# Performance work log

Measured on AMD Instinct MI355X. Metric: run time of the kernel, lower is better.

Reference implementation:

```python
import jax, jax.numpy as jnp
import numpy as np

N_NODES = 100000
N_EDGES = 1600000
MIN_NORM = 1e-15
EPS_F32 = 4e-3  # PoincareBall eps for float32


def _norm(x):
    return jnp.clip(jnp.linalg.norm(x, axis=-1, keepdims=True), MIN_NORM)


def artanh(x):
    x = jnp.clip(x, -1.0 + 1e-15, 1.0 - 1e-15)
    return 0.5 * (jnp.log1p(x) - jnp.log1p(-x))


def proj(x, c):
    norm = _norm(x)
    maxnorm = (1.0 - EPS_F32) / jnp.sqrt(c)
    return jnp.where(norm > maxnorm, x / norm * maxnorm, x)


def expmap0(u, c):
    sqrt_c = jnp.sqrt(c)
    u_norm = _norm(u)
    return jnp.tanh(sqrt_c * u_norm) * u / (sqrt_c * u_norm)


def logmap0(p, c):
    sqrt_c = jnp.sqrt(c)
    p_norm = _norm(p)
    return artanh(sqrt_c * p_norm) * p / (sqrt_c * p_norm)


def mobius_add(x, y, c):
    x2 = jnp.sum(x * x, axis=-1, keepdims=True)
    y2 = jnp.sum(y * y, axis=-1, keepdims=True)
    xy = jnp.sum(x * y, axis=-1, keepdims=True)
    num = (1.0 + 2.0 * c * xy + c * y2) * x + (1.0 - c * x2) * y
    denom = 1.0 + 2.0 * c * xy + (c ** 2) * x2 * y2
    return num / jnp.clip(denom, MIN_NORM)


def mobius_matvec(m, x, c):
    sqrt_c = jnp.sqrt(c)
    x_norm = _norm(x)
    mx = x @ m.T  # [N, out]
    mx_norm = _norm(mx)
    res = jnp.tanh(mx_norm / x_norm * artanh(sqrt_c * x_norm)) * mx / (mx_norm * sqrt_c)
    cond = jnp.all(mx == 0.0, axis=-1, keepdims=True)
    return jnp.where(cond, 0.0, res)


def hyp_linear(x, w, b, c):
    mv = proj(mobius_matvec(w, x, c), c)
    hyp_bias = proj(expmap0(b[None, :], c), c)  # proj_tan0 is identity on Poincare ball
    return proj(mobius_add(mv, hyp_bias, c), c)


def hyp_agg(x, edge_row, edge_col, edge_weight, c):
    x_tan = logmap0(x, c)
    msgs = edge_weight[:, None] * x_tan[edge_col]  # gather source features
    support = jax.ops.segment_sum(msgs, edge_row, num_segments=N_NODES)
    return proj(expmap0(support, c), c)


def hyp_act(x, c_in, c_out):
    xt = jax.nn.relu(logmap0(x, c_in))  # proj_tan0 identity
    return proj(expmap0(xt, c_out), c_out)


def setup_inputs() -> dict:
    key = jax.random.key(0)
    ks = jax.random.split(key, 10)
    x = jax.random.normal(ks[0], (N_NODES, 1433), dtype=jnp.float32)
    edge_row = jax.random.randint(ks[1], (N_EDGES,), 0, N_NODES, dtype=jnp.int32)
    edge_col = jax.random.randint(ks[2], (N_EDGES,), 0, N_NODES, dtype=jnp.int32)
    edge_weight = jax.random.uniform(ks[3], (N_EDGES,), dtype=jnp.float32)
    w1 = jax.random.normal(ks[4], (100, 1433), dtype=jnp.float32) * 0.05
    b1 = jax.random.normal(ks[5], (100,), dtype=jnp.float32) * 0.05
    w2 = jax.random.normal(ks[6], (64, 100), dtype=jnp.float32) * 0.05
    b2 = jax.random.normal(ks[7], (64,), dtype=jnp.float32) * 0.05
    lin_w = jax.random.normal(ks[8], (7, 64), dtype=jnp.float32) * 0.05
    lin_b = jax.random.normal(ks[9], (7,), dtype=jnp.float32) * 0.05
    return {"x": x, "edge_row": edge_row, "edge_col": edge_col,
            "edge_weight": edge_weight, "w1": w1, "b1": b1,
            "w2": w2, "b2": b2, "lin_w": lin_w, "lin_b": lin_b}


def reference(x, edge_row, edge_col, edge_weight, w1, b1, w2, b2, lin_w, lin_b):
    c = 1.0
    # encode: tangent -> hyperbolic (proj_tan0 is identity)
    h = proj(expmap0(x, c), c)
    # layer 1: HypLinear -> HypAgg -> HypAct
    h = hyp_linear(h, w1, b1, c)
    h = hyp_agg(h, edge_row, edge_col, edge_weight, c)
    h = hyp_act(h, c, c)
    # layer 2
    h = hyp_linear(h, w2, b2, c)
    h = hyp_agg(h, edge_row, edge_col, edge_weight, c)
    h = hyp_act(h, c, c)
    # decode: logmap0 -> Linear(64,7) with relu -> log_softmax
    t = logmap0(h, c)
    logits = jax.nn.relu(t @ lin_w.T + lin_b)
    return jax.nn.log_softmax(logits, axis=-1)
```

## Files before the change

kernel.cpp:

```cpp
#include <hip/hip_runtime.h>
#include <hip/hip_bf16.h>
#include <math.h>

#define MINN 1e-15f
#define MAXN 0.996f

#define KPAD 1472

typedef __attribute__((ext_vector_type(8))) short short8;
typedef __attribute__((ext_vector_type(4))) float f32x4;

__device__ __forceinline__ float artanhf_(float v){
  v = fminf(fmaxf(v, -0.9999999f), 0.9999999f);
  return 0.5f*(log1pf(v) - log1pf(-v));
}
__device__ __forceinline__ float grp8(float v){
  v += __shfl_xor(v,1,8); v += __shfl_xor(v,2,8); v += __shfl_xor(v,4,8); return v;
}
__device__ __forceinline__ float grp16w(float v){
  v += __shfl_xor(v,1,16); v += __shfl_xor(v,2,16);
  v += __shfl_xor(v,4,16); v += __shfl_xor(v,8,16); return v;
}
__device__ __forceinline__ unsigned short f2bf(float f){
  unsigned int u = __float_as_uint(f);
  unsigned int r = (u + 0x7fffu + ((u >> 16) & 1u)) >> 16;
  return (unsigned short)r;
}
__device__ __forceinline__ float bf2f(unsigned short h){
  return __uint_as_float(((unsigned int)h) << 16);
}
__device__ __forceinline__ unsigned short f2bf_c(float f){
  __hip_bfloat16 b = __float2bfloat16(f);
  return *reinterpret_cast<unsigned short*>(&b);
}

typedef __attribute__((address_space(1))) const unsigned int gu32;
typedef __attribute__((address_space(3))) unsigned int su32;
__device__ __forceinline__ void gload_lds16(const void* g, void* s){
  __builtin_amdgcn_global_load_lds((gu32*)g, (su32*)s, 16, 0, 0);
}

__global__ __launch_bounds__(256) void k_prep(const float* __restrict__ w1,
    const float* __restrict__ b1, const float* __restrict__ b2,
    unsigned short* __restrict__ w1hi,
    float* __restrict__ hb1, float* __restrict__ hb2, float* __restrict__ scal,
    int* __restrict__ counts, int N){
  int idx = blockIdx.x*256 + threadIdx.x;
  if (idx < 112*KPAD){
    int col = idx / KPAD, k = idx - col*KPAD;
    float v = (col < 100 && k < 1433) ? w1[(size_t)col*1433 + k] : 0.f;
    w1hi[idx] = f2bf(v);
  }
  if (idx < N) counts[idx] = 0;

  if (blockIdx.x == 0){
    __shared__ float red[128];
    int t = threadIdx.x;
    float v = (t < 100) ? b1[t] : 0.f;
    if (t < 128) red[t] = v*v;
    __syncthreads();
    for (int s=64;s;s>>=1){ if (t<s) red[t]+=red[t+s]; __syncthreads(); }
    float n2 = red[0]; __syncthreads();
    float n = fmaxf(sqrtf(n2), MINN);
    float s1 = tanhf(n)/n;
    float pn = fmaxf(tanhf(n), MINN);
    float t1 = pn > MAXN ? MAXN/pn : 1.f;
    float hv = s1*t1*v;
    if (t < 128) hb1[t] = (t<100) ? hv : 0.f;
    if (t < 128) red[t] = (t<100) ? hv*hv : 0.f;
    __syncthreads();
    for (int s=64;s;s>>=1){ if (t<s) red[t]+=red[t+s]; __syncthreads(); }
    if (t==0) scal[0] = red[0];
    __syncthreads();
    float v2 = (t < 64) ? b2[t] : 0.f;
    if (t < 128) red[t] = v2*v2;
    __syncthreads();
    for (int s=64;s;s>>=1){ if (t<s) red[t]+=red[t+s]; __syncthreads(); }
    float n2b = red[0]; __syncthreads();
    float nb = fmaxf(sqrtf(n2b), MINN);
    float s1b = tanhf(nb)/nb;
    float pnb = fmaxf(tanhf(nb), MINN);
    float t1b = pnb > MAXN ? MAXN/pnb : 1.f;
    float hvb = s1b*t1b*v2;
    if (t < 64) hb2[t] = hvb;
    if (t < 128) red[t] = (t<64) ? hvb*hvb : 0.f;
    __syncthreads();
    for (int s=64;s;s>>=1){ if (t<s) red[t]+=red[t+s]; __syncthreads(); }
    if (t==0) scal[1] = red[0];
  }
}

__global__ __launch_bounds__(512) void k_lin1_mfma(
    const float* __restrict__ x, const unsigned short* __restrict__ w1hi,
    const float* __restrict__ hb1,
    const float* __restrict__ scal, unsigned short* __restrict__ xtan1, int N,
    const int* __restrict__ er, int* __restrict__ counts, int E)
{
  __shared__ alignas(16) char bsm[2*14*1024];
  int tid = threadIdx.x;

  {
    int gsz = gridDim.x * 512;
    for (int e = blockIdx.x*512 + tid; e < E; e += gsz)
      atomicAdd(&counts[er[e]], 1);
  }

  int w = tid >> 6, l = tid & 63;
  int lr = l & 15, lg = l >> 4;
  int bm = blockIdx.x * 128;
  int row0 = bm + w*16;
  int r = row0 + lr;
  const float* xr = x + (size_t)min(r, N-1)*1433 + lg*8;
  float b1sq = scal[0];

  f32x4 acc[7];
  #pragma unroll
  for (int t=0;t<7;t++) acc[t] = (f32x4){0.f,0.f,0.f,0.f};
  float sq = 0.f;

  auto stage = [&](int buf, int kbase){
    #pragma unroll
    for (int c = 0; c < 2; ++c){
      int cc = w + 8*c;
      if (cc < 14){
        int h = (cc >= 7) ? 1 : 0;
        int t = cc - h*7;
        const unsigned short* src = w1hi + (size_t)(t*16 + lr)*KPAD + kbase + h*32 + lg*8;
        gload_lds16(src, bsm + (buf*14 + cc)*1024);
      }
    }
  };
  auto xload = [&](float* d, int kbase){
    #pragma unroll
    for (int h = 0; h < 2; ++h){
      int kk = kbase + h*32;
      const float* p = xr + kk;
      if (kk + 32 <= 1433) {
        #pragma unroll
        for (int j=0;j<8;j++) d[h*8+j] = p[j];
      } else {
        #pragma unroll
        for (int j=0;j<8;j++){
          bool kv = (kk + lg*8 + j) < 1433;
          d[h*8+j] = kv ? p[j] : 0.f;
        }
      }
    }
  };

  stage(0, 0);
  float xa[16];
  xload(xa, 0);
  __syncthreads();

  for (int kb = 0; kb < 23; ++kb) {
    int cur = kb & 1, nxt = cur ^ 1;
    int nk = (kb + 1) * 64;

    float xb[16];
    if (kb + 1 < 23){
      stage(nxt, nk);
      xload(xb, nk);
    } else {
      #pragma unroll
      for (int j=0;j<16;j++) xb[j] = 0.f;
    }

    #pragma unroll
    for (int h = 0; h < 2; ++h){
      short8 ah, al;
      #pragma unroll
      for (int j=0;j<8;j++){
        float v = xa[h*8+j];
        sq = fmaf(v, v, sq);
        unsigned short hu = f2bf_c(v);
        ah[j] = (short)hu;
        float hf = bf2f(hu);
        al[j] = (short)f2bf_c(v - hf);
      }
      const char* base = bsm + (cur*14 + h*7)*1024 + (l << 4);
      short8 bh[7];
      #pragma unroll
      for (int t=0;t<7;t++)
        bh[t] = *reinterpret_cast<const short8*>(base + t*1024);
      #pragma unroll
      for (int t=0;t<7;t++){
        acc[t] = __builtin_amdgcn_mfma_f32_16x16x32_bf16(ah, bh[t], acc[t], 0,0,0);
        acc[t] = __builtin_amdgcn_mfma_f32_16x16x32_bf16(al, bh[t], acc[t], 0,0,0);
      }
    }
    #pragma unroll
    for (int j=0;j<16;j++) xa[j] = xb[j];

    __syncthreads();
  }

  sq += __shfl_xor(sq, 16); sq += __shfl_xor(sq, 32);

  float hbv[7];
  #pragma unroll
  for (int t=0;t<7;t++) hbv[t] = hb1[t*16 + lr];

  #pragma unroll
  for (int r4=0;r4<4;r4++){
    int rrow = 4*lg + r4;
    float v[7];
    #pragma unroll
    for (int t=0;t<7;t++) v[t] = acc[t][r4];
    float yn2 = 0.f, dotb = 0.f;
    #pragma unroll
    for (int t=0;t<7;t++){ yn2 += v[t]*v[t]; dotb += v[t]*hbv[t]; }
    yn2 = grp16w(yn2); dotb = grp16w(dotb);
    float xn2 = __shfl(sq, rrow);

    float un = fmaxf(sqrtf(xn2), MINN);
    float th = tanhf(un);
    float sE = th/un;
    float pn = fmaxf(th, MINN);
    float t1 = pn > MAXN ? MAXN/pn : 1.f;
    float gam = sE*t1;
    float xh = fmaxf(gam*un, MINN);
    float yn = sqrtf(yn2);
    float mxn = fmaxf(gam*yn, MINN);
    float rs = tanhf(mxn/xh*artanhf_(xh))/mxn;
    if (yn2 == 0.f) rs = 0.f;
    float rn = rs*gam*yn;
    float t2 = rn > MAXN ? MAXN/fmaxf(rn,MINN) : 1.f;
    float alpha = t2*rs*gam;
    float x2v = alpha*alpha*yn2;
    float xyv = alpha*dotb;
    float den = fmaxf(1.f + 2.f*xyv + x2v*b1sq, MINN);
    float A = (1.f + 2.f*xyv + b1sq)/den, B = (1.f - x2v)/den;
    float Aa = A*alpha;
    float on2 = 0.f;
    float o[7];
    #pragma unroll
    for (int t=0;t<7;t++){ o[t] = Aa*v[t] + B*hbv[t]; on2 += o[t]*o[t]; }
    on2 = grp16w(on2);
    float on = sqrtf(on2);
    float onc = fmaxf(on, MINN);
    float t3 = onc > MAXN ? MAXN/onc : 1.f;
    float pn3 = fmaxf(t3*on, MINN);
    float fs = artanhf_(pn3)/pn3 * t3;

    int grow = row0 + rrow;
    if (grow < N){
      #pragma unroll
      for (int t=0;t<7;t++){
        int c = t*16 + lr;
        if (c < 100) xtan1[(size_t)grow*100 + c] = f2bf(fs*o[t]);
      }
    }
  }
}

__global__ __launch_bounds__(256) void k_scan1(const int* __restrict__ counts, int* __restrict__ row_start,
                                               int* __restrict__ blksum, int N){
  __shared__ int s[256];
  int t = threadIdx.x;
  int base = blockIdx.x*1024 + t*4;
  int v[4]; int sum = 0;
  #pragma unroll
  for (int i=0;i<4;i++){ v[i] = (base+i < N) ? counts[base+i] : 0; sum += v[i]; }
  s[t] = sum; __syncthreads();
  for (int off=1; off<256; off<<=1){
    int val = (t >= off) ? s[t-off] : 0;
    __syncthreads();
    s[t] += val;
    __syncthreads();
  }
  int run = (t > 0) ? s[t-1] : 0;
  #pragma unroll
  for (int i=0;i<4;i++){ if (base+i < N) row_start[base+i] = run; run += v[i]; }
  if (t == 255) blksum[blockIdx.x] = s[255];
}

__global__ __launch_bounds__(256) void k_scan3(int* __restrict__ row_start, const int* __restrict__ blksum,
                                               int* __restrict__ cursor, int N){
  __shared__ int pref;
  if (threadIdx.x == 0){
    int seg = blockIdx.x >> 2;
    int s = 0;
    for (int q = 0; q < seg; ++q) s += blksum[q];
    pref = s;
  }
  __syncthreads();
  int i = blockIdx.x*256 + threadIdx.x;
  if (i < N){ int v = row_start[i] + pref; row_start[i] = v; cursor[i] = v; }
}

__global__ __launch_bounds__(256) void k_scatter(const int* __restrict__ er, const int* __restrict__ ec,
    const float* __restrict__ ew, int* __restrict__ cursor,
    uint2* __restrict__ meta, int E){
  int e = blockIdx.x*256 + threadIdx.x;
  if (e < E){
    int r = er[e];
    int pos = atomicAdd(&cursor[r], 1);
    uint2 m;
    m.x = (unsigned int)ec[e];
    m.y = __float_as_uint(ew[e]);
    meta[pos] = m;
  }
}

__global__ __launch_bounds__(256) void k_agg100(
    const unsigned short* __restrict__ xt, const int* __restrict__ row_start,
    const int* __restrict__ counts, const uint2* __restrict__ meta,
    float* __restrict__ sup, int N)
{
  int row = blockIdx.x*4 + (threadIdx.x >> 6);
  int lane = threadIdx.x & 63;
  if (row >= N) return;
  int start = row_start[row], cnt = counts[row];
  bool act = lane < 50;
  float a0 = 0.f, a1 = 0.f;
  for (int j = 0; j < cnt; j += 64) {
    int cc = 0; float wt = 0.f;
    if (j + lane < cnt) { uint2 m = meta[start + j + lane]; cc = (int)m.x; wt = __uint_as_float(m.y); }
    int lim = min(64, cnt - j);
    int k = 0;
    for (; k + 8 <= lim; k += 8) {
      const unsigned int *p0,*p1,*p2,*p3,*p4,*p5,*p6,*p7;
      float w0,w1,w2,w3,w4,w5,w6,w7;
      p0 = reinterpret_cast<const unsigned int*>(xt + (size_t)__shfl(cc,k+0)*100); w0 = __shfl(wt,k+0);
      p1 = reinterpret_cast<const unsigned int*>(xt + (size_t)__shfl(cc,k+1)*100); w1 = __shfl(wt,k+1);
      p2 = reinterpret_cast<const unsigned int*>(xt + (size_t)__shfl(cc,k+2)*100); w2 = __shfl(wt,k+2);
      p3 = reinterpret_cast<const unsigned int*>(xt + (size_t)__shfl(cc,k+3)*100); w3 = __shfl(wt,k+3);
      p4 = reinterpret_cast<const unsigned int*>(xt + (size_t)__shfl(cc,k+4)*100); w4 = __shfl(wt,k+4);
      p5 = reinterpret_cast<const unsigned int*>(xt + (size_t)__shfl(cc,k+5)*100); w5 = __shfl(wt,k+5);
      p6 = reinterpret_cast<const unsigned int*>(xt + (size_t)__shfl(cc,k+6)*100); w6 = __shfl(wt,k+6);
      p7 = reinterpret_cast<const unsigned int*>(xt + (size_t)__shfl(cc,k+7)*100); w7 = __shfl(wt,k+7);
      if (act){
        unsigned int u0=p0[lane],u1=p1[lane],u2=p2[lane],u3=p3[lane];
        unsigned int u4=p4[lane],u5=p5[lane],u6=p6[lane],u7=p7[lane];
        a0 += w0*bf2f((unsigned short)u0); a1 += w0*bf2f((unsigned short)(u0>>16));
        a0 += w1*bf2f((unsigned short)u1); a1 += w1*bf2f((unsigned short)(u1>>16));
        a0 += w2*bf2f((unsigned short)u2); a1 += w2*bf2f((unsigned short)(u2>>16));
        a0 += w3*bf2f((unsigned short)u3); a1 += w3*bf2f((unsigned short)(u3>>16));
        a0 += w4*bf2f((unsigned short)u4); a1 += w4*bf2f((unsigned short)(u4>>16));
        a0 += w5*bf2f((unsigned short)u5); a1 += w5*bf2f((unsigned short)(u5>>16));
        a0 += w6*bf2f((unsigned short)u6); a1 += w6*bf2f((unsigned short)(u6>>16));
        a0 += w7*bf2f((unsigned short)u7); a1 += w7*bf2f((unsigned short)(u7>>16));
      }
    }
    for (; k < lim; ++k) {
      int col = __shfl(cc, k);
      float w_  = __shfl(wt, k);
      if (act){
        unsigned int u = reinterpret_cast<const unsigned int*>(xt + (size_t)col*100)[lane];
        a0 += w_*bf2f((unsigned short)u);
        a1 += w_*bf2f((unsigned short)(u>>16));
      }
    }
  }
  if (act){
    float2* dst = reinterpret_cast<float2*>(sup + (size_t)row*100);
    dst[lane] = make_float2(a0, a1);
  }
}

__global__ __launch_bounds__(256) void k_agg64(
    const unsigned short* __restrict__ xt, const int* __restrict__ row_start,
    const int* __restrict__ counts, const uint2* __restrict__ meta,
    float* __restrict__ sup, int N)
{
  int row = blockIdx.x*4 + (threadIdx.x >> 6);
  int lane = threadIdx.x & 63;
  if (row >= N) return;
  int half = lane >> 5, sl = lane & 31;
  int start = row_start[row], cnt = counts[row];
  float a0 = 0.f, a1 = 0.f;
  for (int j = 0; j < cnt; j += 64) {
    int cc = 0; float wt = 0.f;
    if (j + lane < cnt) { uint2 m = meta[start + j + lane]; cc = (int)m.x; wt = __uint_as_float(m.y); }
    int lim = min(64, cnt - j);
    int k = 0;
    for (; k + 16 <= lim; k += 16) {
      const unsigned int *p0,*p1,*p2,*p3,*p4,*p5,*p6,*p7;
      float w0,w1,w2,w3,w4,w5,w6,w7;
      p0 = reinterpret_cast<const unsigned int*>(xt + (size_t)__shfl(cc,k+ 0+half)*64); w0 = __shfl(wt,k+ 0+half);
      p1 = reinterpret_cast<const unsigned int*>(xt + (size_t)__shfl(cc,k+ 2+half)*64); w1 = __shfl(wt,k+ 2+half);
      p2 = reinterpret_cast<const unsigned int*>(xt + (size_t)__shfl(cc,k+ 4+half)*64); w2 = __shfl(wt,k+ 4+half);
      p3 = reinterpret_cast<const unsigned int*>(xt + (size_t)__shfl(cc,k+ 6+half)*64); w3 = __shfl(wt,k+ 6+half);
      p4 = reinterpret_cast<const unsigned int*>(xt + (size_t)__shfl(cc,k+ 8+half)*64); w4 = __shfl(wt,k+ 8+half);
      p5 = reinterpret_cast<const unsigned int*>(xt + (size_t)__shfl(cc,k+10+half)*64); w5 = __shfl(wt,k+10+half);
      p6 = reinterpret_cast<const unsigned int*>(xt + (size_t)__shfl(cc,k+12+half)*64); w6 = __shfl(wt,k+12+half);
      p7 = reinterpret_cast<const unsigned int*>(xt + (size_t)__shfl(cc,k+14+half)*64); w7 = __shfl(wt,k+14+half);
      unsigned int u0=p0[sl],u1=p1[sl],u2=p2[sl],u3=p3[sl];
      unsigned int u4=p4[sl],u5=p5[sl],u6=p6[sl],u7=p7[sl];
      a0 += w0*bf2f((unsigned short)u0); a1 += w0*bf2f((unsigned short)(u0>>16));
      a0 += w1*bf2f((unsigned short)u1); a1 += w1*bf2f((unsigned short)(u1>>16));
      a0 += w2*bf2f((unsigned short)u2); a1 += w2*bf2f((unsigned short)(u2>>16));
      a0 += w3*bf2f((unsigned short)u3); a1 += w3*bf2f((unsigned short)(u3>>16));
      a0 += w4*bf2f((unsigned short)u4); a1 += w4*bf2f((unsigned short)(u4>>16));
      a0 += w5*bf2f((unsigned short)u5); a1 += w5*bf2f((unsigned short)(u5>>16));
      a0 += w6*bf2f((unsigned short)u6); a1 += w6*bf2f((unsigned short)(u6>>16));
      a0 += w7*bf2f((unsigned short)u7); a1 += w7*bf2f((unsigned short)(u7>>16));
    }
    for (; k + 2 <= lim; k += 2) {
      int e = k + half;
      int col = __shfl(cc, e);
      float w_ = __shfl(wt, e);
      unsigned int u = reinterpret_cast<const unsigned int*>(xt + (size_t)col*64)[sl];
      a0 += w_*bf2f((unsigned short)u);
      a1 += w_*bf2f((unsigned short)(u>>16));
    }
    if (k < lim) {
      int col = __shfl(cc, k);
      float w_ = __shfl(wt, k);
      if (half == 0){
        unsigned int u = reinterpret_cast<const unsigned int*>(xt + (size_t)col*64)[sl];
        a0 += w_*bf2f((unsigned short)u);
        a1 += w_*bf2f((unsigned short)(u>>16));
      }
    }
  }
  a0 += __shfl_xor(a0, 32);
  a1 += __shfl_xor(a1, 32);
  if (lane < 32){
    float2* dst = reinterpret_cast<float2*>(sup + (size_t)row*64);
    dst[sl] = make_float2(a0, a1);
  }
}

__global__ __launch_bounds__(256) void k_layer2(
    const float* __restrict__ sup, const float* __restrict__ w2,
    const float* __restrict__ hb2, const float* __restrict__ scal,
    unsigned short* __restrict__ xtan2, int N)
{
  __shared__ alignas(16) float w2s[64][100];
  __shared__ float xts[32][105];
  __shared__ float hbs[64];
  int tid = threadIdx.x;
  for (int i = tid; i < 1600; i += 256)
    reinterpret_cast<float4*>(&w2s[0][0])[i] = reinterpret_cast<const float4*>(w2)[i];
  if (tid < 64) hbs[tid] = hb2[tid];
  float b2sq = scal[1];
  __syncthreads();
  int rr = tid >> 3, g = tid & 7;
  int grow = blockIdx.x*32 + rr;
  bool valid = grow < N;
  float sv[13]; float sn2 = 0.f;
  #pragma unroll
  for (int m=0;m<13;m++){
    int j = g + 8*m;
    float v = (valid && j < 100) ? sup[(size_t)grow*100 + j] : 0.f;
    sv[m] = v; sn2 += v*v;
  }
  sn2 = grp8(sn2);
  float snn = fmaxf(sqrtf(sn2), MINN);
  float e1 = tanhf(snn)/snn;
  float pnA = fmaxf(tanhf(snn), MINN);
  float t1 = pnA > MAXN ? MAXN/pnA : 1.f;
  float phi = e1*t1;
  float hn = fmaxf(phi*snn, MINN);
  float lam = artanhf_(hn)/hn;
  float xn2 = 0.f;
  #pragma unroll
  for (int m=0;m<13;m++){
    int j = g + 8*m;
    if (j < 100){ float v = fmaxf(lam*phi*sv[m], 0.f); xts[rr][j] = v; xn2 += v*v; }
  }
  xn2 = grp8(xn2);
  float xn = fmaxf(sqrtf(xn2), MINN);
  float e2 = tanhf(xn)/xn;
  float pnB = fmaxf(tanhf(xn), MINN);
  float t2 = pnB > MAXN ? MAXN/pnB : 1.f;
  float psi = e2*t2;
  __syncthreads();
  float z[8] = {};
  for (int j=0;j<100;j++){
    float xv = xts[rr][j];
    #pragma unroll
    for (int m=0;m<8;m++) z[m] += xv * w2s[g+8*m][j];
  }
  float zn2 = 0.f, dz = 0.f;
  #pragma unroll
  for (int m=0;m<8;m++){ zn2 += z[m]*z[m]; dz += z[m]*hbs[g+8*m]; }
  zn2 = grp8(zn2); dz = grp8(dz);
  float xnh = fmaxf(psi*xn, MINN);
  float zn = sqrtf(zn2);
  float mxn = fmaxf(psi*zn, MINN);
  float rs = tanhf(mxn/xnh*artanhf_(xnh))/mxn;
  if (zn2 == 0.f) rs = 0.f;
  float rn = rs*psi*zn;
  float t3 = rn > MAXN ? MAXN/fmaxf(rn,MINN) : 1.f;
  float alpha = t3*rs*psi;
  float x2 = alpha*alpha*zn2;
  float xy = alpha*dz;
  float den = fmaxf(1.f + 2.f*xy + x2*b2sq, MINN);
  float A = (1.f + 2.f*xy + b2sq)/den, B = (1.f - x2)/den;
  float Aa = A*alpha;
  float ov[8]; float on2 = 0.f;
  #pragma unroll
  for (int m=0;m<8;m++){ ov[m] = Aa*z[m] + B*hbs[g+8*m]; on2 += ov[m]*ov[m]; }
  on2 = grp8(on2);
  float on = sqrtf(on2);
  float onc = fmaxf(on, MINN);
  float t4 = onc > MAXN ? MAXN/onc : 1.f;
  float pn4 = fmaxf(t4*on, MINN);
  float fs = artanhf_(pn4)/pn4 * t4;
  if (valid)
    #pragma unroll
    for (int m=0;m<8;m++) xtan2[(size_t)grow*64 + g + 8*m] = f2bf(fs*ov[m]);
}

__global__ __launch_bounds__(256) void k_decode(
    const float* __restrict__ sup2, const float* __restrict__ lw,
    const float* __restrict__ lb, float* __restrict__ out, int N)
{
  __shared__ float lws[7][64];
  __shared__ float lbs[7];
  int tid = threadIdx.x;
  for (int i = tid; i < 448; i += 256) lws[i>>6][i&63] = lw[i];
  if (tid < 7) lbs[tid] = lb[tid];
  __syncthreads();
  int rr = tid >> 3, g = tid & 7;
  int grow = blockIdx.x*32 + rr;
  bool valid = grow < N;
  float sv[8]; float sn2 = 0.f;
  #pragma unroll
  for (int m=0;m<8;m++){
    int j = g + 8*m;
    float v = valid ? sup2[(size_t)grow*64 + j] : 0.f;
    sv[m] = v; sn2 += v*v;
  }
  sn2 = grp8(sn2);
  float snn = fmaxf(sqrtf(sn2), MINN);
  float e1 = tanhf(snn)/snn;
  float pnA = fmaxf(tanhf(snn), MINN);
  float t1 = pnA > MAXN ? MAXN/pnA : 1.f;
  float phi = e1*t1;
  float hn = fmaxf(phi*snn, MINN);
  float lam = artanhf_(hn)/hn;
  float xt[8]; float xn2 = 0.f;
  #pragma unroll
  for (int m=0;m<8;m++){ xt[m] = fmaxf(lam*phi*sv[m], 0.f); xn2 += xt[m]*xt[m]; }
  xn2 = grp8(xn2);
  float xn = fmaxf(sqrtf(xn2), MINN);
  float e2 = tanhf(xn)/xn;
  float pnB = fmaxf(tanhf(xn), MINN);
  float t2 = pnB > MAXN ? MAXN/pnB : 1.f;
  float psi = e2*t2;
  float tn = fmaxf(psi*xn, MINN);
  float lam2 = artanhf_(tn)/tn;
  float tc = lam2*psi;
  float lg[7];
  #pragma unroll
  for (int k=0;k<7;k++){
    float p = 0.f;
    #pragma unroll
    for (int m=0;m<8;m++) p += xt[m]*lws[k][g+8*m];
    p = grp8(p) * tc;
    lg[k] = fmaxf(p + lbs[k], 0.f);
  }
  float mx = lg[0];
  #pragma unroll
  for (int k=1;k<7;k++) mx = fmaxf(mx, lg[k]);
  float se = 0.f;
  #pragma unroll
  for (int k=0;k<7;k++) se += expf(lg[k]-mx);
  float lse = logf(se);
  if (valid && g < 7) out[(size_t)grow*7 + g] = lg[g] - mx - lse;
}

extern "C" void kernel_launch(void* const* d_in, const int* in_sizes, int n_in,
                              void* d_out, int out_size, void* d_ws, size_t ws_size,
                              hipStream_t stream)
{
  const float* x  = (const float*)d_in[0];
  const int*   er = (const int*)  d_in[1];
  const int*   ec = (const int*)  d_in[2];
  const float* ew = (const float*)d_in[3];
  const float* w1 = (const float*)d_in[4];
  const float* b1 = (const float*)d_in[5];
  const float* w2 = (const float*)d_in[6];
  const float* b2 = (const float*)d_in[7];
  const float* lw = (const float*)d_in[8];
  const float* lb = (const float*)d_in[9];
  float* out = (float*)d_out;
  int N = in_sizes[0] / 1433;
  int E = in_sizes[1];

  float* W = (float*)d_ws;
  float* hb1  = W;
  float* hb2  = W + 128;
  float* scal = W + 192;
  unsigned short* w1hi = (unsigned short*)(W + 256);
  uint2* meta = (uint2*)(W + 82688);
  int*   counts    = (int*)(W + 82688 + 2*(size_t)E);
  int*   row_start = counts + N;
  int*   cursor    = row_start + N;
  int*   blksum    = cursor + N;
  unsigned short* xtanb = (unsigned short*)(blksum + 128);
  float* sup = (float*)(xtanb + (size_t)N*100);

  int nblk_scan = (N + 1023) / 1024;
  int nb128 = (N + 127)/128;
  int nbg = (N + 3)/4;
  int nb32 = (N + 31)/32;

  k_prep<<<(112*KPAD + 255)/256, 256, 0, stream>>>(w1, b1, b2, w1hi, hb1, hb2, scal, counts, N);
  k_lin1_mfma<<<nb128, 512, 0, stream>>>(x, w1hi, hb1, scal, xtanb, N, er, counts, E);
  k_scan1<<<nblk_scan, 256, 0, stream>>>(counts, row_start, blksum, N);
  k_scan3<<<(N + 255)/256, 256, 0, stream>>>(row_start, blksum, cursor, N);
  k_scatter<<<(E + 255)/256, 256, 0, stream>>>(er, ec, ew, cursor, meta, E);
  k_agg100<<<nbg, 256, 0, stream>>>(xtanb, row_start, counts, meta, sup, N);
  k_layer2<<<nb32, 256, 0, stream>>>(sup, w2, hb2, scal, xtanb, N);
  k_agg64<<<nbg, 256, 0, stream>>>(xtanb, row_start, counts, meta, sup, N);
  k_decode<<<nb32, 256, 0, stream>>>(sup, lw, lb, out, N);
}
```

Measured before the change: 577.0 us.

## Process two rows per wavefront in aggregation kernels and reorder GEMM prefetch loads

Both SpMM aggregation kernels now assign two destination rows to each wavefront, with each half-wave loading the edge metadata for one row. The agg64 kernel gives each 32-lane half its own row, which removes the cross-half reduction. The agg100 kernel interleaves gathers for both rows to raise the number of loads in flight. This aims to reduce per-row overhead and improve memory-level parallelism, at the cost of imbalance when the two rows have different degrees. The layer-1 GEMM loop also issues the global x loads before the LDS staging of weights.

```diff
diff --git a/kernel.cpp b/kernel.cpp
--- a/kernel.cpp
+++ b/kernel.cpp
@@ -148,9 +148,9 @@
     }
   };
 
-  stage(0, 0);
   float xa[16];
   xload(xa, 0);
+  stage(0, 0);
   __syncthreads();
 
   for (int kb = 0; kb < 23; ++kb) {
@@ -159,8 +159,8 @@
 
     float xb[16];
     if (kb + 1 < 23){
+      xload(xb, nk);
       stage(nxt, nk);
-      xload(xb, nk);
     } else {
       #pragma unroll
       for (int j=0;j<16;j++) xb[j] = 0.f;
@@ -308,54 +308,81 @@
     const int* __restrict__ counts, const uint2* __restrict__ meta,
     float* __restrict__ sup, int N)
 {
-  int row = blockIdx.x*4 + (threadIdx.x >> 6);
+  int wv = threadIdx.x >> 6;
   int lane = threadIdx.x & 63;
-  if (row >= N) return;
-  int start = row_start[row], cnt = counts[row];
+  int pair = blockIdx.x*4 + wv;
+  int rowA = pair*2;
+  if (rowA >= N) return;
+  int rowB = rowA + 1;
+  bool hasB = rowB < N;
+  int sl = lane & 31, half = lane >> 5;
+  int startA = row_start[rowA], cntA = counts[rowA];
+  int startB = hasB ? row_start[rowB] : 0;
+  int cntB   = hasB ? counts[rowB] : 0;
   bool act = lane < 50;
-  float a0 = 0.f, a1 = 0.f;
-  for (int j = 0; j < cnt; j += 64) {
+  float a0=0.f, a1=0.f, b0=0.f, b1=0.f;
+  int cmax = max(cntA, cntB);
+
+  for (int j = 0; j < cmax; j += 32) {
     int cc = 0; float wt = 0.f;
-    if (j + lane < cnt) { uint2 m = meta[start + j + lane]; cc = (int)m.x; wt = __uint_as_float(m.y); }
-    int lim = min(64, cnt - j);
+    int myStart = half ? startB : startA;
+    int myCnt   = half ? cntB   : cntA;
+    if (j + sl < myCnt){ uint2 m = meta[myStart + j + sl]; cc = (int)m.x; wt = __uint_as_float(m.y); }
+    int limA = min(32, cntA - j);
+    int limB = min(32, cntB - j);
+    int limJ = min(limA, limB);
     int k = 0;
-    for (; k + 8 <= lim; k += 8) {
-      const unsigned int *p0,*p1,*p2,*p3,*p4,*p5,*p6,*p7;
-      float w0,w1,w2,w3,w4,w5,w6,w7;
-      p0 = reinterpret_cast<const unsigned int*>(xt + (size_t)__shfl(cc,k+0)*100); w0 = __shfl(wt,k+0);
-      p1 = reinterpret_cast<const unsigned int*>(xt + (size_t)__shfl(cc,k+1)*100); w1 = __shfl(wt,k+1);
-      p2 = reinterpret_cast<const unsigned int*>(xt + (size_t)__shfl(cc,k+2)*100); w2 = __shfl(wt,k+2);
-      p3 = reinterpret_cast<const unsigned int*>(xt + (size_t)__shfl(cc,k+3)*100); w3 = __shfl(wt,k+3);
-      p4 = reinterpret_cast<const unsigned int*>(xt + (size_t)__shfl(cc,k+4)*100); w4 = __shfl(wt,k+4);
-      p5 = reinterpret_cast<const unsigned int*>(xt + (size_t)__shfl(cc,k+5)*100); w5 = __shfl(wt,k+5);
-      p6 = reinterpret_cast<const unsigned int*>(xt + (size_t)__shfl(cc,k+6)*100); w6 = __shfl(wt,k+6);
-      p7 = reinterpret_cast<const unsigned int*>(xt + (size_t)__shfl(cc,k+7)*100); w7 = __shfl(wt,k+7);
+    for (; k + 4 <= limJ; k += 4) {
+      const unsigned int *pa0,*pa1,*pa2,*pa3,*pb0,*pb1,*pb2,*pb3;
+      float wa0,wa1,wa2,wa3,wb0,wb1,wb2,wb3;
+      pa0 = reinterpret_cast<const unsigned int*>(xt + (size_t)__shfl(cc,k+0)*100); wa0 = __shfl(wt,k+0);
+      pa1 = reinterpret_cast<const unsigned int*>(xt + (size_t)__shfl(cc,k+1)*100); wa1 = __shfl(wt,k+1);
+      pa2 = reinterpret_cast<const unsigned int*>(xt + (size_t)__shfl(cc,k+2)*100); wa2 = __shfl(wt,k+2);
+      pa3 = reinterpret_cast<const unsigned int*>(xt + (size_t)__shfl(cc,k+3)*100); wa3 = __shfl(wt,k+3);
+      pb0 = reinterpret_cast<const unsigned int*>(xt + (size_t)__shfl(cc,32+k+0)*100); wb0 = __shfl(wt,32+k+0);
+      pb1 = reinterpret_cast<const unsigned int*>(xt + (size_t)__shfl(cc,32+k+1)*100); wb1 = __shfl(wt,32+k+1);
+      pb2 = reinterpret_cast<const unsigned int*>(xt + (size_t)__shfl(cc,32+k+2)*100); wb2 = __shfl(wt,32+k+2);
+      pb3 = reinterpret_cast<const unsigned int*>(xt + (size_t)__shfl(cc,32+k+3)*100); wb3 = __shfl(wt,32+k+3);
       if (act){
-        unsigned int u0=p0[lane],u1=p1[lane],u2=p2[lane],u3=p3[lane];
-        unsigned int u4=p4[lane],u5=p5[lane],u6=p6[lane],u7=p7[lane];
-        a0 += w0*bf2f((unsigned short)u0); a1 += w0*bf2f((unsigned short)(u0>>16));
-        a0 += w1*bf2f((unsigned short)u1); a1 += w1*bf2f((unsigned short)(u1>>16));
-        a0 += w2*bf2f((unsigned short)u2); a1 += w2*bf2f((unsigned short)(u2>>16));
-        a0 += w3*bf2f((unsigned short)u3); a1 += w3*bf2f((unsigned short)(u3>>16));
-        a0 += w4*bf2f((unsigned short)u4); a1 += w4*bf2f((unsigned short)(u4>>16));
-        a0 += w5*bf2f((unsigned short)u5); a1 += w5*bf2f((unsigned short)(u5>>16));
-        a0 += w6*bf2f((unsigned short)u6); a1 += w6*bf2f((unsigned short)(u6>>16));
-        a0 += w7*bf2f((unsigned short)u7); a1 += w7*bf2f((unsigned short)(u7>>16));
-      }
-    }
-    for (; k < lim; ++k) {
-      int col = __shfl(cc, k);
-      float w_  = __shfl(wt, k);
+        unsigned int uA0=pa0[lane],uA1=pa1[lane],uA2=pa2[lane],uA3=pa3[lane];
+        unsigned int uB0=pb0[lane],uB1=pb1[lane],uB2=pb2[lane],uB3=pb3[lane];
+        a0 += wa0*bf2f((unsigned short)uA0); a1 += wa0*bf2f((unsigned short)(uA0>>16));
+        a0 += wa1*bf2f((unsigned short)uA1); a1 += wa1*bf2f((unsigned short)(uA1>>16));
+        a0 += wa2*bf2f((unsigned short)uA2); a1 += wa2*bf2f((unsigned short)(uA2>>16));
+        a0 += wa3*bf2f((unsigned short)uA3); a1 += wa3*bf2f((unsigned short)(uA3>>16));
+        b0 += wb0*bf2f((unsigned short)uB0); b1 += wb0*bf2f((unsigned short)(uB0>>16));
+        b0 += wb1*bf2f((unsigned short)uB1); b1 += wb1*bf2f((unsigned short)(uB1>>16));
+        b0 += wb2*bf2f((unsigned short)uB2); b1 += wb2*bf2f((unsigned short)(uB2>>16));
+        b0 += wb3*bf2f((unsigned short)uB3); b1 += wb3*bf2f((unsigned short)(uB3>>16));
+      }
+    }
+    int kA = k, kB = k;
+    for (; kA < limA; ++kA) {
+      int col = __shfl(cc, kA);
+      float w_ = __shfl(wt, kA);
       if (act){
         unsigned int u = reinterpret_cast<const unsigned int*>(xt + (size_t)col*100)[lane];
         a0 += w_*bf2f((unsigned short)u);
         a1 += w_*bf2f((unsigned short)(u>>16));
       }
     }
+    for (; kB < limB; ++kB) {
+      int col = __shfl(cc, 32+kB);
+      float w_ = __shfl(wt, 32+kB);
+      if (act){
+        unsigned int u = reinterpret_cast<const unsigned int*>(xt + (size_t)col*100)[lane];
+        b0 += w_*bf2f((unsigned short)u);
+        b1 += w_*bf2f((unsigned short)(u>>16));
+      }
+    }
   }
   if (act){
-    float2* dst = reinterpret_cast<float2*>(sup + (size_t)row*100);
-    dst[lane] = make_float2(a0, a1);
+    float2* dstA = reinterpret_cast<float2*>(sup + (size_t)rowA*100);
+    dstA[lane] = make_float2(a0, a1);
+    if (hasB){
+      float2* dstB = reinterpret_cast<float2*>(sup + (size_t)rowB*100);
+      dstB[lane] = make_float2(b0, b1);
+    }
   }
 }
 
@@ -364,28 +391,37 @@
     const int* __restrict__ counts, const uint2* __restrict__ meta,
     float* __restrict__ sup, int N)
 {
-  int row = blockIdx.x*4 + (threadIdx.x >> 6);
+  int wv = threadIdx.x >> 6;
   int lane = threadIdx.x & 63;
-  if (row >= N) return;
+  int pair = blockIdx.x*4 + wv;
+  int rowA = pair*2;
+  if (rowA >= N) return;
+  int rowB = rowA + 1;
+  bool hasB = rowB < N;
   int half = lane >> 5, sl = lane & 31;
-  int start = row_start[row], cnt = counts[row];
+  int myRow = half ? rowB : rowA;
+  bool live = (half == 0) || hasB;
+  int myStart = 0, myCnt = 0;
+  if (live){ myStart = row_start[myRow]; myCnt = counts[myRow]; }
   float a0 = 0.f, a1 = 0.f;
-  for (int j = 0; j < cnt; j += 64) {
+
+  for (int j = 0; j < myCnt; j += 32) {
     int cc = 0; float wt = 0.f;
-    if (j + lane < cnt) { uint2 m = meta[start + j + lane]; cc = (int)m.x; wt = __uint_as_float(m.y); }
-    int lim = min(64, cnt - j);
+    if (j + sl < myCnt){ uint2 m = meta[myStart + j + sl]; cc = (int)m.x; wt = __uint_as_float(m.y); }
+    int lim = min(32, myCnt - j);
+    int hb = half*32;
     int k = 0;
-    for (; k + 16 <= lim; k += 16) {
+    for (; k + 8 <= lim; k += 8) {
       const unsigned int *p0,*p1,*p2,*p3,*p4,*p5,*p6,*p7;
       float w0,w1,w2,w3,w4,w5,w6,w7;
-      p0 = reinterpret_cast<const unsigned int*>(xt + (size_t)__shfl(cc,k+ 0+half)*64); w0 = __shfl(wt,k+ 0+half);
-      p1 = reinterpret_cast<const unsigned int*>(xt + (size_t)__shfl(cc,k+ 2+half)*64); w1 = __shfl(wt,k+ 2+half);
-      p2 = reinterpret_cast<const unsigned int*>(xt + (size_t)__shfl(cc,k+ 4+half)*64); w2 = __shfl(wt,k+ 4+half);
-      p3 = reinterpret_cast<const unsigned int*>(xt + (size_t)__shfl(cc,k+ 6+half)*64); w3 = __shfl(wt,k+ 6+half);
-      p4 = reinterpret_cast<const unsigned int*>(xt + (size_t)__shfl(cc,k+ 8+half)*64); w4 = __shfl(wt,k+ 8+half);
-      p5 = reinterpret_cast<const unsigned int*>(xt + (size_t)__shfl(cc,k+10+half)*64); w5 = __shfl(wt,k+10+half);
-      p6 = reinterpret_cast<const unsigned int*>(xt + (size_t)__shfl(cc,k+12+half)*64); w6 = __shfl(wt,k+12+half);
-      p7 = reinterpret_cast<const unsigned int*>(xt + (size_t)__shfl(cc,k+14+half)*64); w7 = __shfl(wt,k+14+half);
+      p0 = reinterpret_cast<const unsigned int*>(xt + (size_t)__shfl(cc,hb+k+0)*64); w0 = __shfl(wt,hb+k+0);
+      p1 = reinterpret_cast<const unsigned int*>(xt + (size_t)__shfl(cc,hb+k+1)*64); w1 = __shfl(wt,hb+k+1);
+      p2 = reinterpret_cast<const unsigned int*>(xt + (size_t)__shfl(cc,hb+k+2)*64); w2 = __shfl(wt,hb+k+2);
+      p3 = reinterpret_cast<const unsigned int*>(xt + (size_t)__shfl(cc,hb+k+3)*64); w3 = __shfl(wt,hb+k+3);
+      p4 = reinterpret_cast<const unsigned int*>(xt + (size_t)__shfl(cc,hb+k+4)*64); w4 = __shfl(wt,hb+k+4);
+      p5 = reinterpret_cast<const unsigned int*>(xt + (size_t)__shfl(cc,hb+k+5)*64); w5 = __shfl(wt,hb+k+5);
+      p6 = reinterpret_cast<const unsigned int*>(xt + (size_t)__shfl(cc,hb+k+6)*64); w6 = __shfl(wt,hb+k+6);
+      p7 = reinterpret_cast<const unsigned int*>(xt + (size_t)__shfl(cc,hb+k+7)*64); w7 = __shfl(wt,hb+k+7);
       unsigned int u0=p0[sl],u1=p1[sl],u2=p2[sl],u3=p3[sl];
       unsigned int u4=p4[sl],u5=p5[sl],u6=p6[sl],u7=p7[sl];
       a0 += w0*bf2f((unsigned short)u0); a1 += w0*bf2f((unsigned short)(u0>>16));
@@ -397,28 +433,16 @@
       a0 += w6*bf2f((unsigned short)u6); a1 += w6*bf2f((unsigned short)(u6>>16));
       a0 += w7*bf2f((unsigned short)u7); a1 += w7*bf2f((unsigned short)(u7>>16));
     }
-    for (; k + 2 <= lim; k += 2) {
-      int e = k + half;
-      int col = __shfl(cc, e);
-      float w_ = __shfl(wt, e);
+    for (; k < lim; ++k) {
+      int col = __shfl(cc, hb+k);
+      float w_ = __shfl(wt, hb+k);
       unsigned int u = reinterpret_cast<const unsigned int*>(xt + (size_t)col*64)[sl];
       a0 += w_*bf2f((unsigned short)u);
       a1 += w_*bf2f((unsigned short)(u>>16));
     }
-    if (k < lim) {
-      int col = __shfl(cc, k);
-      float w_ = __shfl(wt, k);
-      if (half == 0){
-        unsigned int u = reinterpret_cast<const unsigned int*>(xt + (size_t)col*64)[sl];
-        a0 += w_*bf2f((unsigned short)u);
-        a1 += w_*bf2f((unsigned short)(u>>16));
-      }
-    }
-  }
-  a0 += __shfl_xor(a0, 32);
-  a1 += __shfl_xor(a1, 32);
-  if (lane < 32){
-    float2* dst = reinterpret_cast<float2*>(sup + (size_t)row*64);
+  }
+  if (live){
+    float2* dst = reinterpret_cast<float2*>(sup + (size_t)myRow*64);
     dst[sl] = make_float2(a0, a1);
   }
 }
@@ -597,7 +621,8 @@
 
   int nblk_scan = (N + 1023) / 1024;
   int nb128 = (N + 127)/128;
-  int nbg = (N + 3)/4;
+  int npair = (N + 1)/2;
+  int nbg = (npair + 3)/4;
   int nb32 = (N + 31)/32;
 
   k_prep<<<(112*KPAD + 255)/256, 256, 0, stream>>>(w1, b1, b2, w1hi, hb1, hb2, scal, counts, N);
```

Measured after the change: 561.9 us (median of 2 runs). -2.6%, faster.
